# Kernel optimization log

Measured on AMD Instinct MI355X. Metric: run time of the kernel, lower is better.

## Reference

```python
import jax, jax.numpy as jnp
import numpy as np

D_MODEL = 2048
NUM_HEADS = 16
HEAD_DIM = D_MODEL // NUM_HEADS
SCALE = HEAD_DIM ** -0.5
ALPHA = 1.0


def setup_inputs() -> dict:
    key = jax.random.key(0)
    ks = jax.random.split(key, 9)
    B, T = 2, 2048
    s = 0.02
    w = lambda k: jax.random.normal(k, (D_MODEL, D_MODEL), jnp.float32) * s
    b = lambda k: jax.random.normal(k, (D_MODEL,), jnp.float32) * s
    return {
        'x': jax.random.normal(ks[0], (B, T, D_MODEL), jnp.float32),
        'q_w': w(ks[1]), 'q_b': b(ks[2]),
        'k_w': w(ks[3]), 'k_b': b(ks[4]),
        'v_w': w(ks[5]), 'v_b': b(ks[6]),
        'o_w': w(ks[7]), 'o_b': b(ks[8]),
    }


def reference(x, q_w, q_b, k_w, k_b, v_w, v_b, o_w, o_b):
    B, T, D = x.shape
    H, HD = NUM_HEADS, HEAD_DIM

    def proj_split(w, bias):
        y = x @ w.T + bias  # torch Linear: x @ W^T + b
        # B T (H D) -> (B H) T D
        return y.reshape(B, T, H, HD).transpose(0, 2, 1, 3).reshape(B * H, T, HD)

    Q = proj_split(q_w, q_b)
    K = proj_split(k_w, k_b)
    V = proj_split(v_w, v_b)

    # Note: original computes S[h,i,j] = K_i . Q_j (K first, Q second)
    S = jnp.einsum('hid,hjd->hij', K, Q) * SCALE  # (B*H, T, T)

    idx = jnp.arange(T)
    delta = idx[:, None] - idx[None, :]  # delta[i,j] = i - j
    # similarity_power_law decay: -(delta**alpha) for delta>=0, else 0
    decay = jnp.where(delta < 0, 0.0, -(delta.astype(jnp.float32) ** ALPHA))
    # causal mask: positions with j > i (delta < 0) set to -inf, then add decay
    S = jnp.where(delta < 0, -jnp.inf, S) + decay

    C = jax.nn.softmax(S, axis=-1)
    attn = jnp.einsum('hij,hjd->hid', C, V)  # (B*H, T, HD)
    # (B H) T D -> B T (H D)
    attn = attn.reshape(B, H, T, HD).transpose(0, 2, 1, 3).reshape(B, T, D)
    return attn @ o_w.T + o_b
```

## Files before the change

### kernel.cpp

```cpp
#include <hip/hip_runtime.h>
#include <hip/hip_bf16.h>
#include <stdint.h>

#define BT    4096
#define DM    2048
#define TSEQ  2048
#define NHEAD 16
#define HD    128
#define QKV_LD 6144
#define ATT_SCALE 0.088388347648318447f
#define WIN   64

typedef __attribute__((ext_vector_type(8))) short short8;
typedef __attribute__((ext_vector_type(4))) float f32x4;

__device__ __forceinline__ uint16_t f2bf(float f) {
  uint32_t u = __float_as_uint(f);
  return (uint16_t)((u + 0x7FFFu + ((u >> 16) & 1u)) >> 16);
}

__device__ __forceinline__ void gload_lds16(const void* g, void* l) {
  __builtin_amdgcn_global_load_lds((__attribute__((address_space(1))) void*)g,
                                   (__attribute__((address_space(3))) void*)l,
                                   16, 0, 0);
}

__global__ __launch_bounds__(256) void prep(const float* __restrict__ x,
                                            const float* __restrict__ qw,
                                            const float* __restrict__ kw,
                                            const float* __restrict__ vw,
                                            const float* __restrict__ ow,
                                            const float* __restrict__ qb,
                                            const float* __restrict__ kb,
                                            const float* __restrict__ vb,
                                            uint16_t* __restrict__ xb,
                                            uint16_t* __restrict__ wqkv,
                                            uint16_t* __restrict__ wo,
                                            float* __restrict__ bcat) {
  const int NX = BT * DM / 4;
  const int NW = DM * DM / 4;
  const int total = NX + 4 * NW;
  int i0 = blockIdx.x * 256 + threadIdx.x;
  for (int idx = i0; idx < total; idx += gridDim.x * 256) {
    const float* src;
    uint16_t* dst;
    int off;
    if (idx < NX)            { src = x;  dst = xb;                          off = idx; }
    else if (idx < NX + NW)  { src = qw; dst = wqkv;                        off = idx - NX; }
    else if (idx < NX + 2*NW){ src = kw; dst = wqkv + (size_t)DM * DM;      off = idx - NX - NW; }
    else if (idx < NX + 3*NW){ src = vw; dst = wqkv + (size_t)2 * DM * DM;  off = idx - NX - 2*NW; }
    else                     { src = ow; dst = wo;                          off = idx - NX - 3*NW; }
    float4 v = ((const float4*)src)[off];
    ushort4 o;
    o.x = f2bf(v.x); o.y = f2bf(v.y); o.z = f2bf(v.z); o.w = f2bf(v.w);
    ((ushort4*)dst)[off] = o;
  }
  if (i0 < 3 * DM) {
    float v = (i0 < DM) ? qb[i0] : (i0 < 2 * DM ? kb[i0 - DM] : vb[i0 - 2 * DM]);
    bcat[i0] = v;
  }
}

template <bool OUT_BF16>
__global__ __launch_bounds__(512, 2) void gemm_p4(const uint16_t* __restrict__ A,
                                                  const uint16_t* __restrict__ B,
                                                  const float* __restrict__ bias,
                                                  void* __restrict__ Cout,
                                                  int M, int N, int K) {
  __shared__ uint16_t sm[49152];

  const int tid = threadIdx.x;
  const int l   = tid & 63;
  const int wid = tid >> 6;
  const int wr  = wid >> 2;
  const int wc  = wid & 3;
  const int ln  = l & 15;
  const int g   = l >> 4;

  const int nbx = N >> 8;
  const int nwg = nbx * (M >> 7);
  const int bid = blockIdx.x;
  const int swz = (bid & 7) * (nwg >> 3) + (bid >> 3);
  const int m0  = (swz / nbx) << 7;
  const int n0  = (swz % nbx) << 8;

  const int srow = l >> 2;
  const int gch  = (l & 3) ^ ((l >> 3) & 3);
  const uint16_t* pa  = A + (size_t)(m0 + wid * 16 + srow) * K + gch * 8;
  const uint16_t* pb0 = B + (size_t)(n0 + wid * 16 + srow) * K + gch * 8;
  const uint16_t* pb1 = B + (size_t)(n0 + 128 + wid * 16 + srow) * K + gch * 8;
  const int ldsA  = wid * 512;
  const int ldsB0 = 4096 + wid * 512;
  const int ldsB1 = 8192 + wid * 512;

  const int pc = g ^ ((ln >> 1) & 3);

  f32x4 acc[4][4];
#pragma unroll
  for (int i = 0; i < 4; ++i)
#pragma unroll
    for (int j = 0; j < 4; ++j) acc[i][j] = (f32x4){0.f, 0.f, 0.f, 0.f};

  const int nt = K >> 5;

#define STAGE(T)                                                        \
  {                                                                     \
    uint16_t* base_ = sm + (size_t)((T) & 3) * 12288;                   \
    const size_t ko_ = (size_t)(T) * 32;                                \
    gload_lds16(pa + ko_,  base_ + ldsA);                               \
    gload_lds16(pb0 + ko_, base_ + ldsB0);                              \
    gload_lds16(pb1 + ko_, base_ + ldsB1);                              \
  }

#define COMPUTE(T)                                                      \
  {                                                                     \
    const uint16_t* buf_ = sm + (size_t)((T) & 3) * 12288;              \
    short8 af_[4], bf_[4];                                              \
    _Pragma("unroll")                                                   \
    for (int fi = 0; fi < 4; ++fi)                                      \
      af_[fi] = *(const short8*)(buf_ + (wr * 64 + fi * 16 + ln) * 32 + pc * 8); \
    _Pragma("unroll")                                                   \
    for (int fj = 0; fj < 4; ++fj)                                      \
      bf_[fj] = *(const short8*)(buf_ + 4096 + (wc * 64 + fj * 16 + ln) * 32 + pc * 8); \
    __builtin_amdgcn_s_setprio(1);                                      \
    _Pragma("unroll")                                                   \
    for (int fi = 0; fi < 4; ++fi)                                      \
      _Pragma("unroll")                                                 \
      for (int fj = 0; fj < 4; ++fj)                                    \
        acc[fi][fj] = __builtin_amdgcn_mfma_f32_16x16x32_bf16(          \
            af_[fi], bf_[fj], acc[fi][fj], 0, 0, 0);                    \
    __builtin_amdgcn_s_setprio(0);                                      \
  }

  STAGE(0); STAGE(1); STAGE(2);
  asm volatile("s_waitcnt vmcnt(6)" ::: "memory");
  __builtin_amdgcn_s_barrier();

#pragma unroll 1
  for (int t = 0; t < nt - 3; ++t) {
    STAGE(t + 3);
    COMPUTE(t);
    asm volatile("s_waitcnt vmcnt(6)" ::: "memory");
    __builtin_amdgcn_s_barrier();
  }
  COMPUTE(nt - 3);
  asm volatile("s_waitcnt vmcnt(3)" ::: "memory");
  __builtin_amdgcn_s_barrier();
  COMPUTE(nt - 2);
  asm volatile("s_waitcnt vmcnt(0)" ::: "memory");
  __builtin_amdgcn_s_barrier();
  COMPUTE(nt - 1);
#undef STAGE
#undef COMPUTE

  const int g4 = g * 4;
#pragma unroll
  for (int fi = 0; fi < 4; ++fi) {
    size_t row = (size_t)(m0 + wr * 64 + fi * 16 + g4);
#pragma unroll
    for (int fj = 0; fj < 4; ++fj) {
      int col = n0 + wc * 64 + fj * 16 + ln;
      float bv = bias[col];
#pragma unroll
      for (int r = 0; r < 4; ++r) {
        float v = acc[fi][fj][r] + bv;
        if (OUT_BF16) ((uint16_t*)Cout)[(row + r) * N + col] = f2bf(v);
        else          ((float*)Cout)[(row + r) * N + col] = v;
      }
    }
  }
}

__global__ __launch_bounds__(256) void attn_mfma(const uint16_t* __restrict__ QKV,
                                                 uint16_t* __restrict__ O) {
  __shared__ __align__(16) uint16_t smem[16384 + 17408];
  uint16_t* Qs = smem;
  uint16_t* Vt = smem + 16384;
  uint16_t* Pl = smem;

  const int tid  = threadIdx.x;
  const int lane = tid & 63;
  const int w    = tid >> 6;
  const int g    = lane >> 4;
  const int ln   = lane & 15;

  const int i0 = blockIdx.x * 64;
  const int h  = blockIdx.y;
  const int b  = blockIdx.z;
  const int wb = i0 - 63;
  const size_t hoff  = (size_t)h * HD;
  const size_t bbase = (size_t)b * TSEQ;

#pragma unroll
  for (int it = 0; it < 8; ++it) {
    int s   = it * 256 + tid;
    int row = s >> 4, c = s & 15;
    int j = wb + row;
    if (j >= 0 && j < TSEQ) {
      const uint16_t* gsrc = QKV + (bbase + j) * (size_t)QKV_LD + hoff
                           + (size_t)((c ^ (row & 7)) * 8);
      uint16_t* ldst = Qs + (size_t)(s & ~63) * 8;
      gload_lds16(gsrc, ldst);
    } else {
      uint4 z = {0, 0, 0, 0};
      *(uint4*)(Qs + (size_t)s * 8) = z;
    }
  }

#pragma unroll
  for (int it = 0; it < 4; ++it) {
    int s  = it * 256 + tid;
    int jp = (s & 15) | (it << 4);
    int dc = (s >> 4) & 15;
    int j0 = wb + 2 * jp;
    uint4 va = {0, 0, 0, 0}, vb = {0, 0, 0, 0};
    if (j0 >= 0 && j0 < TSEQ)
      va = *(const uint4*)(QKV + (bbase + j0) * (size_t)QKV_LD + 2 * DM + hoff + dc * 8);
    if (j0 + 1 >= 0 && j0 + 1 < TSEQ)
      vb = *(const uint4*)(QKV + (bbase + j0 + 1) * (size_t)QKV_LD + 2 * DM + hoff + dc * 8);
    const uint16_t* ap = (const uint16_t*)&va;
    const uint16_t* bp = (const uint16_t*)&vb;
#pragma unroll
    for (int t = 0; t < 8; ++t) {
      uint32_t pk = (uint32_t)ap[t] | ((uint32_t)bp[t] << 16);
      *(uint32_t*)(Vt + (size_t)(dc * 8 + t) * 136 + 2 * jp) = pk;
    }
  }

  short8 kreg[4];
  {
    const uint16_t* kp = QKV + (bbase + i0 + w * 16 + ln) * (size_t)QKV_LD
                       + DM + hoff + g * 8;
#pragma unroll
    for (int kc = 0; kc < 4; ++kc) kreg[kc] = *(const short8*)(kp + kc * 32);
  }

  __syncthreads();

  f32x4 acc[8];
#pragma unroll
  for (int nf = 0; nf < 8; ++nf) acc[nf] = (f32x4){0.f, 0.f, 0.f, 0.f};
#pragma unroll
  for (int kc = 0; kc < 4; ++kc) {
#pragma unroll
    for (int nf = 0; nf < 8; ++nf) {
      int row = nf * 16 + ln;
      int chunk = (kc * 4 + g) ^ (row & 7);
      short8 qf = *(const short8*)(Qs + (size_t)row * 128 + chunk * 8);
      acc[nf] = __builtin_amdgcn_mfma_f32_16x16x32_bf16(kreg[kc], qf, acc[nf], 0, 0, 0);
    }
  }

#pragma unroll
  for (int nf = 0; nf < 8; ++nf) {
    int rj = nf * 16 + ln;
    int jg = wb + rj;
#pragma unroll
    for (int r = 0; r < 4; ++r) {
      int il = w * 16 + g * 4 + r;
      int delta = il + 63 - rj;
      float v = acc[nf][r] * ATT_SCALE - (float)delta;
      acc[nf][r] = ((unsigned)delta < 64u && jg >= 0) ? v : -1e30f;
    }
  }

  float inv[4];
#pragma unroll
  for (int r = 0; r < 4; ++r) {
    float mx = acc[0][r];
#pragma unroll
    for (int nf = 1; nf < 8; ++nf) mx = fmaxf(mx, acc[nf][r]);
    mx = fmaxf(mx, __shfl_xor(mx, 1));
    mx = fmaxf(mx, __shfl_xor(mx, 2));
    mx = fmaxf(mx, __shfl_xor(mx, 4));
    mx = fmaxf(mx, __shfl_xor(mx, 8));
    float s = 0.f;
#pragma unroll
    for (int nf = 0; nf < 8; ++nf) {
      float e = __expf(acc[nf][r] - mx);
      acc[nf][r] = e;
      s += e;
    }
    s += __shfl_xor(s, 1);
    s += __shfl_xor(s, 2);
    s += __shfl_xor(s, 4);
    s += __shfl_xor(s, 8);
    inv[r] = 1.0f / s;
  }

  __syncthreads();

#pragma unroll
  for (int nf = 0; nf < 8; ++nf)
#pragma unroll
    for (int r = 0; r < 4; ++r)
      Pl[(size_t)(w * 16 + g * 4 + r) * 136 + nf * 16 + ln] = f2bf(acc[nf][r]);
  asm volatile("s_waitcnt lgkmcnt(0)" ::: "memory");
  __builtin_amdgcn_sched_barrier(0);

  f32x4 o[8];
#pragma unroll
  for (int nf = 0; nf < 8; ++nf) o[nf] = (f32x4){0.f, 0.f, 0.f, 0.f};
#pragma unroll
  for (int kc = 0; kc < 4; ++kc) {
    short8 pa = *(const short8*)(Pl + (size_t)(w * 16 + ln) * 136 + kc * 32 + g * 8);
#pragma unroll
    for (int nf = 0; nf < 8; ++nf) {
      short8 vbf = *(const short8*)(Vt + (size_t)(nf * 16 + ln) * 136 + kc * 32 + g * 8);
      o[nf] = __builtin_amdgcn_mfma_f32_16x16x32_bf16(pa, vbf, o[nf], 0, 0, 0);
    }
  }

  const size_t obase = (bbase + i0 + w * 16) * (size_t)DM + hoff;
#pragma unroll
  for (int nf = 0; nf < 8; ++nf)
#pragma unroll
    for (int r = 0; r < 4; ++r)
      O[obase + (size_t)(g * 4 + r) * DM + nf * 16 + ln] = f2bf(o[nf][r] * inv[r]);
}

extern "C" void kernel_launch(void* const* d_in, const int* in_sizes, int n_in,
                              void* d_out, int out_size, void* d_ws, size_t ws_size,
                              hipStream_t stream) {
  const float* x   = (const float*)d_in[0];
  const float* q_w = (const float*)d_in[1];
  const float* q_b = (const float*)d_in[2];
  const float* k_w = (const float*)d_in[3];
  const float* k_b = (const float*)d_in[4];
  const float* v_w = (const float*)d_in[5];
  const float* v_b = (const float*)d_in[6];
  const float* o_w = (const float*)d_in[7];
  const float* o_b = (const float*)d_in[8];

  char* ws = (char*)d_ws;
  const size_t XB_BYTES   = (size_t)BT * DM * 2;
  const size_t W_BYTES    = (size_t)DM * DM * 2;
  const size_t WQKV_BYTES = 3 * W_BYTES;

  uint16_t* xb   = (uint16_t*)(ws);
  uint16_t* wqkv = (uint16_t*)(ws + XB_BYTES);
  uint16_t* wo   = (uint16_t*)(ws + XB_BYTES + WQKV_BYTES);
  float*    bcat = (float*)   (ws + XB_BYTES + WQKV_BYTES + W_BYTES);
  uint16_t* QKVb = (uint16_t*)(ws + XB_BYTES + WQKV_BYTES + W_BYTES + 24576);

  prep<<<2048, 256, 0, stream>>>(x, q_w, k_w, v_w, o_w, q_b, k_b, v_b,
                                 xb, wqkv, wo, bcat);

  gemm_p4<true><<<(BT / 128) * (3 * DM / 256), 512, 0, stream>>>(
      xb, wqkv, bcat, QKVb, BT, 3 * DM, DM);

  dim3 ga(TSEQ / 64, NHEAD, 2);
  attn_mfma<<<ga, 256, 0, stream>>>(QKVb, xb);

  gemm_p4<false><<<(BT / 128) * (DM / 256), 512, 0, stream>>>(
      xb, wo, o_b, d_out, BT, DM, DM);
}
```

Measured before the change: 206.7 us.

## Use 256x256 tiles for QKV GEMM with XCD-rectangle block mapping

Templates the GEMM on the M-fragment count so the QKV projection uses 256x256 output tiles (8x4 MFMA fragments per wave), loading two A sub-tiles per stage and adjusting the vmcnt waits to match. It also replaces the block swizzle with a mapping that gives each XCD a rectangular region of tiles, aiming to improve L2 reuse. The larger tile cuts global and LDS traffic per flop, but it raises register and LDS use. Launch bounds drop to one block per CU, which lowers occupancy and halves the QKV grid to 384 blocks.

```diff
diff --git a/kernel.cpp b/kernel.cpp
--- a/kernel.cpp
+++ b/kernel.cpp
@@ -61,13 +61,18 @@
   }
 }
 
-template <bool OUT_BF16>
-__global__ __launch_bounds__(512, 2) void gemm_p4(const uint16_t* __restrict__ A,
+template <int MF, bool OUT_BF16>
+__global__ __launch_bounds__(512, 1) void gemm_p4(const uint16_t* __restrict__ A,
                                                   const uint16_t* __restrict__ B,
                                                   const float* __restrict__ bias,
                                                   void* __restrict__ Cout,
                                                   int M, int N, int K) {
-  __shared__ uint16_t sm[49152];
+  constexpr int BM   = MF * 32;
+  constexpr int ABUF = BM * 32;
+  constexpr int BUFE = ABUF + 8192;
+  constexpr int MB   = (MF == 8) ? 2 : 4;
+  constexpr int NB   = 8 / MB;
+  __shared__ uint16_t sm[4 * BUFE];
 
   const int tid = threadIdx.x;
   const int l   = tid & 63;
@@ -77,12 +82,16 @@
   const int ln  = l & 15;
   const int g   = l >> 4;
 
-  const int nbx = N >> 8;
-  const int nwg = nbx * (M >> 7);
-  const int bid = blockIdx.x;
-  const int swz = (bid & 7) * (nwg >> 3) + (bid >> 3);
-  const int m0  = (swz / nbx) << 7;
-  const int n0  = (swz % nbx) << 8;
+  const int nbx    = N >> 8;
+  const int bid    = blockIdx.x;
+  const int xcd    = bid & 7;
+  const int idx    = bid >> 3;
+  const int rect_n = nbx / NB;
+  const int rect_m = (M / BM) / MB;
+  const int m_t    = (xcd / NB) * rect_m + idx / rect_n;
+  const int n_t    = (xcd % NB) * rect_n + idx % rect_n;
+  const int m0     = m_t * BM;
+  const int n0     = n_t << 8;
 
   const int srow = l >> 2;
   const int gch  = (l & 3) ^ ((l >> 3) & 3);
@@ -90,14 +99,14 @@
   const uint16_t* pb0 = B + (size_t)(n0 + wid * 16 + srow) * K + gch * 8;
   const uint16_t* pb1 = B + (size_t)(n0 + 128 + wid * 16 + srow) * K + gch * 8;
   const int ldsA  = wid * 512;
-  const int ldsB0 = 4096 + wid * 512;
-  const int ldsB1 = 8192 + wid * 512;
+  const int ldsB0 = ABUF + wid * 512;
+  const int ldsB1 = ABUF + 4096 + wid * 512;
 
   const int pc = g ^ ((ln >> 1) & 3);
 
-  f32x4 acc[4][4];
-#pragma unroll
-  for (int i = 0; i < 4; ++i)
+  f32x4 acc[MF][4];
+#pragma unroll
+  for (int i = 0; i < MF; ++i)
 #pragma unroll
     for (int j = 0; j < 4; ++j) acc[i][j] = (f32x4){0.f, 0.f, 0.f, 0.f};
 
@@ -105,26 +114,27 @@
 
 #define STAGE(T)                                                        \
   {                                                                     \
-    uint16_t* base_ = sm + (size_t)((T) & 3) * 12288;                   \
+    uint16_t* base_ = sm + (size_t)((T) & 3) * BUFE;                    \
     const size_t ko_ = (size_t)(T) * 32;                                \
-    gload_lds16(pa + ko_,  base_ + ldsA);                               \
+    gload_lds16(pa + ko_, base_ + ldsA);                                \
+    if (MF == 8) gload_lds16(pa + (size_t)128 * K + ko_, base_ + 4096 + ldsA); \
     gload_lds16(pb0 + ko_, base_ + ldsB0);                              \
     gload_lds16(pb1 + ko_, base_ + ldsB1);                              \
   }
 
 #define COMPUTE(T)                                                      \
   {                                                                     \
-    const uint16_t* buf_ = sm + (size_t)((T) & 3) * 12288;              \
-    short8 af_[4], bf_[4];                                              \
+    const uint16_t* buf_ = sm + (size_t)((T) & 3) * BUFE;               \
+    short8 af_[MF], bf_[4];                                             \
     _Pragma("unroll")                                                   \
-    for (int fi = 0; fi < 4; ++fi)                                      \
-      af_[fi] = *(const short8*)(buf_ + (wr * 64 + fi * 16 + ln) * 32 + pc * 8); \
+    for (int fi = 0; fi < MF; ++fi)                                     \
+      af_[fi] = *(const short8*)(buf_ + (wr * (MF * 16) + fi * 16 + ln) * 32 + pc * 8); \
     _Pragma("unroll")                                                   \
     for (int fj = 0; fj < 4; ++fj)                                      \
-      bf_[fj] = *(const short8*)(buf_ + 4096 + (wc * 64 + fj * 16 + ln) * 32 + pc * 8); \
+      bf_[fj] = *(const short8*)(buf_ + ABUF + (wc * 64 + fj * 16 + ln) * 32 + pc * 8); \
     __builtin_amdgcn_s_setprio(1);                                      \
     _Pragma("unroll")                                                   \
-    for (int fi = 0; fi < 4; ++fi)                                      \
+    for (int fi = 0; fi < MF; ++fi)                                     \
       _Pragma("unroll")                                                 \
       for (int fj = 0; fj < 4; ++fj)                                    \
         acc[fi][fj] = __builtin_amdgcn_mfma_f32_16x16x32_bf16(          \
@@ -132,19 +142,26 @@
     __builtin_amdgcn_s_setprio(0);                                      \
   }
 
+#define WAIT_LOOP()                                                     \
+  if (MF == 8) asm volatile("s_waitcnt vmcnt(8)" ::: "memory");         \
+  else         asm volatile("s_waitcnt vmcnt(6)" ::: "memory");
+#define WAIT_PEEL1()                                                    \
+  if (MF == 8) asm volatile("s_waitcnt vmcnt(4)" ::: "memory");         \
+  else         asm volatile("s_waitcnt vmcnt(3)" ::: "memory");
+
   STAGE(0); STAGE(1); STAGE(2);
-  asm volatile("s_waitcnt vmcnt(6)" ::: "memory");
+  WAIT_LOOP();
   __builtin_amdgcn_s_barrier();
 
 #pragma unroll 1
   for (int t = 0; t < nt - 3; ++t) {
     STAGE(t + 3);
     COMPUTE(t);
-    asm volatile("s_waitcnt vmcnt(6)" ::: "memory");
+    WAIT_LOOP();
     __builtin_amdgcn_s_barrier();
   }
   COMPUTE(nt - 3);
-  asm volatile("s_waitcnt vmcnt(3)" ::: "memory");
+  WAIT_PEEL1();
   __builtin_amdgcn_s_barrier();
   COMPUTE(nt - 2);
   asm volatile("s_waitcnt vmcnt(0)" ::: "memory");
@@ -152,11 +169,13 @@
   COMPUTE(nt - 1);
 #undef STAGE
 #undef COMPUTE
+#undef WAIT_LOOP
+#undef WAIT_PEEL1
 
   const int g4 = g * 4;
 #pragma unroll
-  for (int fi = 0; fi < 4; ++fi) {
-    size_t row = (size_t)(m0 + wr * 64 + fi * 16 + g4);
+  for (int fi = 0; fi < MF; ++fi) {
+    size_t row = (size_t)(m0 + wr * (MF * 16) + fi * 16 + g4);
 #pragma unroll
     for (int fj = 0; fj < 4; ++fj) {
       int col = n0 + wc * 64 + fj * 16 + ln;
@@ -346,12 +365,12 @@
   prep<<<2048, 256, 0, stream>>>(x, q_w, k_w, v_w, o_w, q_b, k_b, v_b,
                                  xb, wqkv, wo, bcat);
 
-  gemm_p4<true><<<(BT / 128) * (3 * DM / 256), 512, 0, stream>>>(
+  gemm_p4<8, true><<<(BT / 256) * (3 * DM / 256), 512, 0, stream>>>(
       xb, wqkv, bcat, QKVb, BT, 3 * DM, DM);
 
   dim3 ga(TSEQ / 64, NHEAD, 2);
   attn_mfma<<<ga, 256, 0, stream>>>(QKVb, xb);
 
-  gemm_p4<false><<<(BT / 128) * (DM / 256), 512, 0, stream>>>(
+  gemm_p4<4, false><<<(BT / 128) * (DM / 256), 512, 0, stream>>>(
       xb, wo, o_b, d_out, BT, DM, DM);
 }
```

New measurement: 202.7 us. About the same (-1.9%).

## Switch GEMMs to 128x128 tiles with 4 waves and XCD-aware rectangle mapping

Applied to the files above, without the earlier changes.

Replaces the 128x256-tile, 512-thread GEMM with a 128x128-tile, 256-thread variant that issues four LDS loads per stage. The block-to-tile mapping now assigns each of the eight XCDs a contiguous rectangle of output tiles so that tiles sharing A or B rows land on the same L2. The aim is better L2 reuse and more workgroups to fill the CUs. In exchange, each tile has less reuse per load and the global-to-LDS traffic per FLOP goes up.

```diff
diff --git a/kernel.cpp b/kernel.cpp
--- a/kernel.cpp
+++ b/kernel.cpp
@@ -61,37 +61,45 @@
   }
 }
 
-template <bool OUT_BF16>
-__global__ __launch_bounds__(512, 2) void gemm_p4(const uint16_t* __restrict__ A,
+template <int MB_, bool OUT_BF16>
+__global__ __launch_bounds__(256, 2) void gemm128(const uint16_t* __restrict__ A,
                                                   const uint16_t* __restrict__ B,
                                                   const float* __restrict__ bias,
                                                   void* __restrict__ Cout,
                                                   int M, int N, int K) {
-  __shared__ uint16_t sm[49152];
+  __shared__ uint16_t sm[4 * 8192];
 
   const int tid = threadIdx.x;
   const int l   = tid & 63;
   const int wid = tid >> 6;
-  const int wr  = wid >> 2;
-  const int wc  = wid & 3;
+  const int wr  = wid >> 1;
+  const int wc  = wid & 1;
   const int ln  = l & 15;
   const int g   = l >> 4;
 
-  const int nbx = N >> 8;
-  const int nwg = nbx * (M >> 7);
-  const int bid = blockIdx.x;
-  const int swz = (bid & 7) * (nwg >> 3) + (bid >> 3);
-  const int m0  = (swz / nbx) << 7;
-  const int n0  = (swz % nbx) << 8;
+  constexpr int NB_ = 8 / MB_;
+  const int nbx    = N >> 7;
+  const int nbm    = M >> 7;
+  const int bid    = blockIdx.x;
+  const int xcd    = bid & 7;
+  const int idx    = bid >> 3;
+  const int rect_n = nbx / NB_;
+  const int rect_m = nbm / MB_;
+  const int m_t    = (xcd / NB_) * rect_m + idx / rect_n;
+  const int n_t    = (xcd % NB_) * rect_n + idx % rect_n;
+  const int m0     = m_t << 7;
+  const int n0     = n_t << 7;
 
   const int srow = l >> 2;
   const int gch  = (l & 3) ^ ((l >> 3) & 3);
-  const uint16_t* pa  = A + (size_t)(m0 + wid * 16 + srow) * K + gch * 8;
+  const uint16_t* pa0 = A + (size_t)(m0 + wid * 16 + srow) * K + gch * 8;
+  const uint16_t* pa1 = pa0 + (size_t)64 * K;
   const uint16_t* pb0 = B + (size_t)(n0 + wid * 16 + srow) * K + gch * 8;
-  const uint16_t* pb1 = B + (size_t)(n0 + 128 + wid * 16 + srow) * K + gch * 8;
-  const int ldsA  = wid * 512;
-  const int ldsB0 = 4096 + wid * 512;
-  const int ldsB1 = 8192 + wid * 512;
+  const uint16_t* pb1 = pb0 + (size_t)64 * K;
+  const int la0 = wid * 512;
+  const int la1 = 2048 + wid * 512;
+  const int lb0 = 4096 + wid * 512;
+  const int lb1 = 6144 + wid * 512;
 
   const int pc = g ^ ((ln >> 1) & 3);
 
@@ -105,16 +113,17 @@
 
 #define STAGE(T)                                                        \
   {                                                                     \
-    uint16_t* base_ = sm + (size_t)((T) & 3) * 12288;                   \
+    uint16_t* base_ = sm + (size_t)((T) & 3) * 8192;                    \
     const size_t ko_ = (size_t)(T) * 32;                                \
-    gload_lds16(pa + ko_,  base_ + ldsA);                               \
-    gload_lds16(pb0 + ko_, base_ + ldsB0);                              \
-    gload_lds16(pb1 + ko_, base_ + ldsB1);                              \
+    gload_lds16(pa0 + ko_, base_ + la0);                                \
+    gload_lds16(pa1 + ko_, base_ + la1);                                \
+    gload_lds16(pb0 + ko_, base_ + lb0);                                \
+    gload_lds16(pb1 + ko_, base_ + lb1);                                \
   }
 
 #define COMPUTE(T)                                                      \
   {                                                                     \
-    const uint16_t* buf_ = sm + (size_t)((T) & 3) * 12288;              \
+    const uint16_t* buf_ = sm + (size_t)((T) & 3) * 8192;               \
     short8 af_[4], bf_[4];                                              \
     _Pragma("unroll")                                                   \
     for (int fi = 0; fi < 4; ++fi)                                      \
@@ -133,18 +142,18 @@
   }
 
   STAGE(0); STAGE(1); STAGE(2);
-  asm volatile("s_waitcnt vmcnt(6)" ::: "memory");
+  asm volatile("s_waitcnt vmcnt(8)" ::: "memory");
   __builtin_amdgcn_s_barrier();
 
 #pragma unroll 1
   for (int t = 0; t < nt - 3; ++t) {
     STAGE(t + 3);
     COMPUTE(t);
-    asm volatile("s_waitcnt vmcnt(6)" ::: "memory");
+    asm volatile("s_waitcnt vmcnt(8)" ::: "memory");
     __builtin_amdgcn_s_barrier();
   }
   COMPUTE(nt - 3);
-  asm volatile("s_waitcnt vmcnt(3)" ::: "memory");
+  asm volatile("s_waitcnt vmcnt(4)" ::: "memory");
   __builtin_amdgcn_s_barrier();
   COMPUTE(nt - 2);
   asm volatile("s_waitcnt vmcnt(0)" ::: "memory");
@@ -346,12 +355,12 @@
   prep<<<2048, 256, 0, stream>>>(x, q_w, k_w, v_w, o_w, q_b, k_b, v_b,
                                  xb, wqkv, wo, bcat);
 
-  gemm_p4<true><<<(BT / 128) * (3 * DM / 256), 512, 0, stream>>>(
+  gemm128<2, true><<<(BT / 128) * (3 * DM / 128), 256, 0, stream>>>(
       xb, wqkv, bcat, QKVb, BT, 3 * DM, DM);
 
   dim3 ga(TSEQ / 64, NHEAD, 2);
   attn_mfma<<<ga, 256, 0, stream>>>(QKVb, xb);
 
-  gemm_p4<false><<<(BT / 128) * (DM / 256), 512, 0, stream>>>(
+  gemm128<4, false><<<(BT / 128) * (DM / 128), 256, 0, stream>>>(
       xb, wo, o_b, d_out, BT, DM, DM);
 }
```

Result: no change. 209.3 us (+1.2%).
